# Kernel optimization log

Measured on AMD Instinct MI355X. Metric: run time of the kernel, lower is better.

## Reference

```python
import jax, jax.numpy as jnp
import numpy as np

NUM_HEADS = 4
KEY_DIM = 64
D_MODEL = 256
OUTPUT_DIM = 256


def setup_inputs() -> dict:
    key = jax.random.key(0)
    ks = jax.random.split(key, 11)
    B, T, D = 16, 1024, D_MODEL
    HD = NUM_HEADS * KEY_DIM
    s = 0.02
    return {
        "query": jax.random.normal(ks[0], (B, T, D), jnp.float32),
        "key": jax.random.normal(ks[1], (B, T, D), jnp.float32),
        "value": jax.random.normal(ks[2], (B, T, D), jnp.float32),
        "Wq": jax.random.normal(ks[3], (D, HD), jnp.float32) * s,
        "bq": jnp.zeros((HD,), jnp.float32),
        "Wk": jax.random.normal(ks[4], (D, HD), jnp.float32) * s,
        "bk": jnp.zeros((HD,), jnp.float32),
        "Wv": jax.random.normal(ks[5], (D, KEY_DIM), jnp.float32) * s,
        "bv": jnp.zeros((KEY_DIM,), jnp.float32),
        "Wo": jax.random.normal(ks[6], (HD, OUTPUT_DIM), jnp.float32) * s,
        "bo": jnp.zeros((OUTPUT_DIM,), jnp.float32),
    }


def reference(query, key, value, Wq, bq, Wk, bk, Wv, bv, Wo, bo):
    B, Tq, _ = query.shape
    Tk = key.shape[1]
    H, Dk = NUM_HEADS, KEY_DIM
    # projections
    q = (query @ Wq + bq).reshape(B, Tq, H, Dk)  # [B,Tq,H,Dk]
    k = (key @ Wk + bk).reshape(B, Tk, H, Dk)    # [B,Tk,H,Dk]
    v = value @ Wv + bv                           # [B,Tk,Dk] shared across heads
    scale = jnp.asarray(Dk, q.dtype) ** -0.5
    # scores [B,H,Tq,Tk]
    score = jnp.einsum("bqhd,bkhd->bhqk", q, k) * scale
    attn = jax.nn.softmax(score, axis=-1)
    # broadcast-V attention: [B,H,Tq,Tk] x [B,Tk,Dk] -> [B,H,Tq,Dk]
    out = jnp.einsum("bhqk,bkd->bhqd", attn, v)
    out = out.transpose(0, 2, 1, 3).reshape(B, Tq, H * Dk)
    return out @ Wo + bo
```

## Files before the change

### kernel.cpp

```cpp
#include <hip/hip_runtime.h>
#include <hip/hip_bf16.h>


typedef __attribute__((ext_vector_type(8))) short short8;
typedef __attribute__((ext_vector_type(4))) float f32x4;
typedef __attribute__((ext_vector_type(16))) float f32x16;

__device__ __forceinline__ short f2bf(float x) {
    return __builtin_bit_cast(short, __float2bfloat16(x));
}

__device__ __forceinline__ float exp2_fast(float x) {
#if __has_builtin(__builtin_amdgcn_exp2f)
    return __builtin_amdgcn_exp2f(x);
#else
    float r; asm("v_exp_f32 %0, %1" : "=v"(r) : "v"(x)); return r;
#endif
}

__device__ __forceinline__ f32x4 mfma16(short8 a, short8 b, f32x4 c) {
    return __builtin_amdgcn_mfma_f32_16x16x32_bf16(a, b, c, 0, 0, 0);
}
__device__ __forceinline__ f32x16 mfma32(short8 a, short8 b, f32x16 c) {
    return __builtin_amdgcn_mfma_f32_32x32x16_bf16(a, b, c, 0, 0, 0);
}

__device__ __forceinline__ int cvtpk(float lo, float hi) {
    int r; asm("v_cvt_pk_bf16_f32 %0, %1, %2" : "=v"(r) : "v"(lo), "v"(hi));
    return r;
}
__device__ __forceinline__ void swap32(int& a, int& b) {
    asm("v_permlane32_swap_b32 %0, %1" : "+v"(a), "+v"(b));
}

__device__ __forceinline__ short8 half_frag(const f32x16& s, int base) {
    int d0 = cvtpk(s[base + 0], s[base + 1]);
    int d1 = cvtpk(s[base + 2], s[base + 3]);
    int d2 = cvtpk(s[base + 4], s[base + 5]);
    int d3 = cvtpk(s[base + 6], s[base + 7]);
    swap32(d0, d2);
    swap32(d1, d3);
    int4 v = { d0, d1, d2, d3 };
    return __builtin_bit_cast(short8, v);
}

#define QSCALE 0.18033688011112042f

__global__ void prep_weights(const float* __restrict__ Wq, const float* __restrict__ Wk,
                             const float* __restrict__ Wv, const float* __restrict__ Wo,
                             short* __restrict__ WqtF, short* __restrict__ WktF,
                             short* __restrict__ WvtF, short* __restrict__ WotF) {
    int tid = blockIdx.x * 256 + threadIdx.x;
    int k = tid >> 8, n = tid & 255;
    int off = ((n >> 6) << 14) + (((n >> 4) & 3) << 12) + ((k >> 5) << 9)
            + (((k >> 3) & 3) << 7) + ((n & 15) << 3) + (k & 7);
    WqtF[off] = f2bf(Wq[k * 256 + n] * QSCALE);
    WktF[off] = f2bf(Wk[k * 256 + n]);
    int offo = ((n >> 5) << 13) + ((k >> 4) << 9) + (((k & 15) >> 3) << 8)
             + ((n & 31) << 3) + (k & 7);
    WotF[offo] = f2bf(Wo[k * 256 + n]);
    if (n < 64) {
        int offv = ((n >> 4) << 12) + ((k >> 5) << 9) + (((k >> 3) & 3) << 7)
                 + ((n & 15) << 3) + (k & 7);
        WvtF[offv] = f2bf(Wv[k * 64 + n]);
    }
}

__global__ __launch_bounds__(256) void proj_all(
        const float* __restrict__ query, const float* __restrict__ key_,
        const float* __restrict__ value,
        const short* __restrict__ WqtF, const short* __restrict__ WktF,
        const short* __restrict__ WvtF,
        const float* __restrict__ bq, const float* __restrict__ bk,
        const float* __restrict__ bv,
        short* __restrict__ qf, short* __restrict__ kf, short* __restrict__ vf) {
    __shared__ short At[8192];
    const int tid = threadIdx.x;
    const int lane = tid & 63, wave = tid >> 6;
    const int u = lane >> 4, r16 = lane & 15;
    const int m0 = blockIdx.x * 32;
    const int task = blockIdx.y;

    const float* A = task == 0 ? query : (task == 1 ? key_ : value);

    #pragma unroll
    for (int j = 0; j < 4; ++j) {
        int p8 = j * 8 + ((wave >> 1) << 2) + u;
        int row = ((wave & 1) << 4) + r16;
        const float* src = A + (m0 + row) * 256 + p8 * 8;
        float4 a0 = *(const float4*)src;
        float4 a1 = *(const float4*)(src + 4);
        short8 w;
        w[0] = f2bf(a0.x); w[1] = f2bf(a0.y); w[2] = f2bf(a0.z); w[3] = f2bf(a0.w);
        w[4] = f2bf(a1.x); w[5] = f2bf(a1.y); w[6] = f2bf(a1.z); w[7] = f2bf(a1.w);
        int dst = ((p8 >> 2) << 10) + ((wave & 1) << 9) + ((p8 & 3) << 7) + (r16 << 3);
        *(short8*)&At[dst] = w;
    }

    const int b = m0 >> 10, t32 = (m0 >> 5) & 31;

    if (task < 2) {
        const short* WtF = task == 0 ? WqtF : WktF;
        const float* bias = task == 0 ? bq : bk;
        const float bscale = task == 0 ? QSCALE : 1.0f;
        short* outF = task == 0 ? qf : kf;
        const short* wb = WtF + (wave << 14);

        short8 bf8[4];
        #pragma unroll
        for (int g = 0; g < 4; ++g) bf8[g] = *(const short8*)&wb[(g << 12) + lane * 8];
        __syncthreads();

        f32x4 acc[2][4] = {};
        #pragma unroll
        for (int kk = 0; kk < 8; ++kk) {
            short8 af[2], nb[4];
            #pragma unroll
            for (int f = 0; f < 2; ++f) af[f] = *(const short8*)&At[(kk << 10) + (f << 9) + lane * 8];
            if (kk < 7) {
                #pragma unroll
                for (int g = 0; g < 4; ++g) nb[g] = *(const short8*)&wb[(g << 12) + ((kk + 1) << 9) + lane * 8];
            }
            #pragma unroll
            for (int f = 0; f < 2; ++f)
                #pragma unroll
                for (int g = 0; g < 4; ++g)
                    acc[f][g] = mfma16(af[f], bf8[g], acc[f][g]);
            #pragma unroll
            for (int g = 0; g < 4; ++g) bf8[g] = nb[g];
        }

        float bvv[4];
        #pragma unroll
        for (int g = 0; g < 4; ++g) bvv[g] = bias[(wave << 6) + 16 * g + r16] * bscale;
        short* ob = outF + ((((b << 2) + wave) << 5) + t32) * 2048;
        #pragma unroll
        for (int f = 0; f < 2; ++f)
            #pragma unroll
            for (int g = 0; g < 4; ++g)
                #pragma unroll
                for (int rr = 0; rr < 4; ++rr)
                    ob[(g << 9) + ((r16 >> 3) << 8) + (16 * f + 4 * u + rr) * 8 + (r16 & 7)]
                        = f2bf(acc[f][g][rr] + bvv[g]);
    } else {
        const int fr = wave >> 1;
        short8 bf8[2];
        #pragma unroll
        for (int z = 0; z < 2; ++z) {
            int dg = ((wave & 1) << 1) + z;
            bf8[z] = *(const short8*)&WvtF[(dg << 12) + lane * 8];
        }
        __syncthreads();

        f32x4 acc[2] = {};
        #pragma unroll
        for (int kk = 0; kk < 8; ++kk) {
            short8 af = *(const short8*)&At[(kk << 10) + (fr << 9) + lane * 8];
            short8 nb[2];
            if (kk < 7) {
                #pragma unroll
                for (int z = 0; z < 2; ++z) {
                    int dg = ((wave & 1) << 1) + z;
                    nb[z] = *(const short8*)&WvtF[(dg << 12) + ((kk + 1) << 9) + lane * 8];
                }
            }
            #pragma unroll
            for (int z = 0; z < 2; ++z) acc[z] = mfma16(af, bf8[z], acc[z]);
            bf8[0] = nb[0]; bf8[1] = nb[1];
        }

        short* ob = vf + ((b << 5) + t32) * 2048;
        #pragma unroll
        for (int z = 0; z < 2; ++z) {
            int dg = ((wave & 1) << 1) + z;
            float bvv = bv[16 * dg + r16];
            #pragma unroll
            for (int rr = 0; rr < 4; ++rr) {
                int tl = 4 * u + rr;
                ob[((dg >> 1) << 10) + (fr << 9) + ((tl >> 3) << 8)
                   + ((16 * (dg & 1) + r16) << 3) + (tl & 7)]
                    = f2bf(acc[z][rr] + bvv);
            }
        }
    }
}

__global__ __launch_bounds__(256, 3) void attn_og(const short* __restrict__ qF,
        const short* __restrict__ kF, const short* __restrict__ vF,
        const short* __restrict__ WoF, const float* __restrict__ bo,
        float* __restrict__ outp) {
    __shared__ short At[8192];
    const int tid = threadIdx.x;
    const int lane = tid & 63, h = tid >> 6;
    const int u2 = lane >> 5, n31 = lane & 31;

    const int L = (blockIdx.x & 7) * 64 + (blockIdx.x >> 3);
    const int b = L >> 5, qt = L & 31;

    const short* qb = qF + ((((b << 2) + h) << 5) + qt) * 2048;
    short8 Q[4];
    #pragma unroll
    for (int c = 0; c < 4; ++c) Q[c] = *(const short8*)&qb[(c << 9) + lane * 8];

    const short* kb = kF + (((b << 2) + h) << 5) * 2048;
    const short* vb = vF + (b << 5) * 2048;

    short8 kfr[4], vfr[4];
    #pragma unroll
    for (int c = 0; c < 4; ++c) {
        kfr[c] = *(const short8*)&kb[(c << 9) + lane * 8];
        vfr[c] = *(const short8*)&vb[(c << 9) + lane * 8];
    }

    f32x16 accO0 = {}, accO1 = {};
    float l = 0.f;

    for (int kt = 0; kt < 32; ++kt) {
        short8 nk[4], nv[4];
        if (kt < 31) {
            const short* kn = kb + (kt + 1) * 2048;
            const short* vn = vb + (kt + 1) * 2048;
            #pragma unroll
            for (int c = 0; c < 4; ++c) {
                nk[c] = *(const short8*)&kn[(c << 9) + lane * 8];
                nv[c] = *(const short8*)&vn[(c << 9) + lane * 8];
            }
        }

        f32x16 S = {};
        __builtin_amdgcn_s_setprio(1);
        S = mfma32(kfr[0], Q[0], S);
        S = mfma32(kfr[1], Q[1], S);
        S = mfma32(kfr[2], Q[2], S);
        S = mfma32(kfr[3], Q[3], S);
        __builtin_amdgcn_s_setprio(0);

        f32x16 E;
        #pragma unroll
        for (int j = 0; j < 16; ++j) E[j] = exp2_fast(S[j]);
        l += (((E[0] + E[1]) + (E[2] + E[3])) + ((E[4] + E[5]) + (E[6] + E[7])))
           + (((E[8] + E[9]) + (E[10] + E[11])) + ((E[12] + E[13]) + (E[14] + E[15])));

        short8 p0 = half_frag(E, 0);
        short8 p1 = half_frag(E, 8);

        __builtin_amdgcn_s_setprio(1);
        accO0 = mfma32(vfr[0], p0, accO0);
        accO0 = mfma32(vfr[1], p1, accO0);
        accO1 = mfma32(vfr[2], p0, accO1);
        accO1 = mfma32(vfr[3], p1, accO1);
        __builtin_amdgcn_s_setprio(0);

        #pragma unroll
        for (int c = 0; c < 4; ++c) { kfr[c] = nk[c]; vfr[c] = nv[c]; }
    }

    l += __shfl_xor(l, 32);
    float linv = 1.0f / l;

    f32x16 O0, O1;
    #pragma unroll
    for (int j = 0; j < 16; ++j) { O0[j] = accO0[j] * linv; O1[j] = accO1[j] * linv; }
    {
        short8 a0 = half_frag(O0, 0), a1 = half_frag(O0, 8);
        short8 a2 = half_frag(O1, 0), a3 = half_frag(O1, 8);
        *(short8*)&At[((4 * h + 0) << 9) + lane * 8] = a0;
        *(short8*)&At[((4 * h + 1) << 9) + lane * 8] = a1;
        *(short8*)&At[((4 * h + 2) << 9) + lane * 8] = a2;
        *(short8*)&At[((4 * h + 3) << 9) + lane * 8] = a3;
    }
    __syncthreads();

    const short* wo0 = WoF + (2 * h) * 8192;
    const short* wo1 = wo0 + 8192;
    f32x16 acc2[2] = {};
    #pragma unroll
    for (int kc = 0; kc < 16; ++kc) {
        short8 a = *(const short8*)&At[(kc << 9) + lane * 8];
        short8 w0 = *(const short8*)&wo0[(kc << 9) + lane * 8];
        short8 w1 = *(const short8*)&wo1[(kc << 9) + lane * 8];
        acc2[0] = mfma32(a, w0, acc2[0]);
        acc2[1] = mfma32(a, w1, acc2[1]);
    }

    const int m0 = L << 5;
    #pragma unroll
    for (int nt2 = 0; nt2 < 2; ++nt2) {
        float bvv = bo[(2 * h + nt2) * 32 + n31];
        #pragma unroll
        for (int r = 0; r < 16; ++r) {
            int q = (r & 3) + 8 * (r >> 2) + 4 * u2;
            outp[(m0 + q) * 256 + (2 * h + nt2) * 32 + n31] = acc2[nt2][r] + bvv;
        }
    }
}

extern "C" void kernel_launch(void* const* d_in, const int* in_sizes, int n_in,
                              void* d_out, int out_size, void* d_ws, size_t ws_size,
                              hipStream_t stream) {
    (void)in_sizes; (void)n_in; (void)out_size; (void)ws_size;
    const float* query = (const float*)d_in[0];
    const float* key_  = (const float*)d_in[1];
    const float* value = (const float*)d_in[2];
    const float* Wq = (const float*)d_in[3];
    const float* bq = (const float*)d_in[4];
    const float* Wk = (const float*)d_in[5];
    const float* bk = (const float*)d_in[6];
    const float* Wv = (const float*)d_in[7];
    const float* bv = (const float*)d_in[8];
    const float* Wo = (const float*)d_in[9];
    const float* bo = (const float*)d_in[10];
    float* outp = (float*)d_out;

    short* wsp  = (short*)d_ws;
    short* WqtF = wsp;
    short* WktF = wsp + 65536;
    short* WotF = wsp + 131072;
    short* WvtF = wsp + 196608;
    short* qf   = wsp + 212992;
    short* kf   = wsp + 4407296;
    short* vf   = wsp + 8601600;

    hipLaunchKernelGGL(prep_weights, dim3(256), dim3(256), 0, stream,
                       Wq, Wk, Wv, Wo, WqtF, WktF, WvtF, WotF);
    hipLaunchKernelGGL(proj_all, dim3(512, 3), dim3(256), 0, stream,
                       query, key_, value, WqtF, WktF, WvtF, bq, bk, bv, qf, kf, vf);
    hipLaunchKernelGGL(attn_og, dim3(512), dim3(256), 0, stream,
                       qf, kf, vf, WotF, bo, outp);
}
```

Baseline: 55.29 us.

## Split KV range across wave pairs and process two query tiles per wave

Each block now covers 64 query rows with 512 threads. Every head gets two waves that each handle half of the key/value sequence over both query tiles, so each K/V fragment load feeds twice as many MFMAs. The partial outputs and row sums are merged through shared memory before the output projection, which is then split across all 8 waves. The cost is more LDS (about 100KB per block), an extra barrier and reduction step, and fewer blocks (256 instead of 512), which may leave many CUs underused. Softmax still uses no running max, as before.

```diff
diff --git a/kernel.cpp b/kernel.cpp
--- a/kernel.cpp
+++ b/kernel.cpp
@@ -42,6 +42,11 @@
     swap32(d1, d3);
     int4 v = { d0, d1, d2, d3 };
     return __builtin_bit_cast(short8, v);
+}
+
+__device__ __forceinline__ float sum16(const f32x16& e) {
+    return (((e[0] + e[1]) + (e[2] + e[3])) + ((e[4] + e[5]) + (e[6] + e[7])))
+         + (((e[8] + e[9]) + (e[10] + e[11])) + ((e[12] + e[13]) + (e[14] + e[15])));
 }
 
 #define QSCALE 0.18033688011112042f
@@ -185,25 +190,31 @@
     }
 }
 
-__global__ __launch_bounds__(256, 3) void attn_og(const short* __restrict__ qF,
+__global__ __launch_bounds__(512, 2) void attn_og(const short* __restrict__ qF,
         const short* __restrict__ kF, const short* __restrict__ vF,
         const short* __restrict__ WoF, const float* __restrict__ bo,
         float* __restrict__ outp) {
-    __shared__ short At[8192];
+    __shared__ float ocm[16384];
+    __shared__ float lcm[512];
+    __shared__ short At[16384];
     const int tid = threadIdx.x;
-    const int lane = tid & 63, h = tid >> 6;
+    const int lane = tid & 63, wave = tid >> 6;
+    const int h = wave >> 1, kvh = wave & 1;
     const int u2 = lane >> 5, n31 = lane & 31;
 
-    const int L = (blockIdx.x & 7) * 64 + (blockIdx.x >> 3);
-    const int b = L >> 5, qt = L & 31;
-
-    const short* qb = qF + ((((b << 2) + h) << 5) + qt) * 2048;
-    short8 Q[4];
+    const int L = (blockIdx.x & 7) * 32 + (blockIdx.x >> 3);
+    const int b = L >> 4, qt = L & 15;
+
+    const short* qb = qF + ((((b << 2) + h) << 5) + (qt << 1)) * 2048;
+    short8 Q0[4], Q1[4];
     #pragma unroll
-    for (int c = 0; c < 4; ++c) Q[c] = *(const short8*)&qb[(c << 9) + lane * 8];
-
-    const short* kb = kF + (((b << 2) + h) << 5) * 2048;
-    const short* vb = vF + (b << 5) * 2048;
+    for (int c = 0; c < 4; ++c) {
+        Q0[c] = *(const short8*)&qb[(c << 9) + lane * 8];
+        Q1[c] = *(const short8*)&qb[2048 + (c << 9) + lane * 8];
+    }
+
+    const short* kb = kF + ((((b << 2) + h) << 5) + (kvh << 4)) * 2048;
+    const short* vb = vF + (((b << 5) + (kvh << 4))) * 2048;
 
     short8 kfr[4], vfr[4];
     #pragma unroll
@@ -212,14 +223,14 @@
         vfr[c] = *(const short8*)&vb[(c << 9) + lane * 8];
     }
 
-    f32x16 accO0 = {}, accO1 = {};
-    float l = 0.f;
-
-    for (int kt = 0; kt < 32; ++kt) {
+    f32x16 aO00 = {}, aO01 = {}, aO10 = {}, aO11 = {};
+    float l0 = 0.f, l1 = 0.f;
+
+    for (int i = 0; i < 16; ++i) {
         short8 nk[4], nv[4];
-        if (kt < 31) {
-            const short* kn = kb + (kt + 1) * 2048;
-            const short* vn = vb + (kt + 1) * 2048;
+        if (i < 15) {
+            const short* kn = kb + (i + 1) * 2048;
+            const short* vn = vb + (i + 1) * 2048;
             #pragma unroll
             for (int c = 0; c < 4; ++c) {
                 nk[c] = *(const short8*)&kn[(c << 9) + lane * 8];
@@ -227,70 +238,119 @@
             }
         }
 
-        f32x16 S = {};
+        f32x16 S0 = {}, S1 = {};
         __builtin_amdgcn_s_setprio(1);
-        S = mfma32(kfr[0], Q[0], S);
-        S = mfma32(kfr[1], Q[1], S);
-        S = mfma32(kfr[2], Q[2], S);
-        S = mfma32(kfr[3], Q[3], S);
+        S0 = mfma32(kfr[0], Q0[0], S0); S1 = mfma32(kfr[0], Q1[0], S1);
+        S0 = mfma32(kfr[1], Q0[1], S0); S1 = mfma32(kfr[1], Q1[1], S1);
+        S0 = mfma32(kfr[2], Q0[2], S0); S1 = mfma32(kfr[2], Q1[2], S1);
+        S0 = mfma32(kfr[3], Q0[3], S0); S1 = mfma32(kfr[3], Q1[3], S1);
         __builtin_amdgcn_s_setprio(0);
 
-        f32x16 E;
-        #pragma unroll
-        for (int j = 0; j < 16; ++j) E[j] = exp2_fast(S[j]);
-        l += (((E[0] + E[1]) + (E[2] + E[3])) + ((E[4] + E[5]) + (E[6] + E[7])))
-           + (((E[8] + E[9]) + (E[10] + E[11])) + ((E[12] + E[13]) + (E[14] + E[15])));
-
-        short8 p0 = half_frag(E, 0);
-        short8 p1 = half_frag(E, 8);
+        #pragma unroll
+        for (int j = 0; j < 16; ++j) S0[j] = exp2_fast(S0[j]);
+        #pragma unroll
+        for (int j = 0; j < 16; ++j) S1[j] = exp2_fast(S1[j]);
+        l0 += sum16(S0);
+        l1 += sum16(S1);
+
+        short8 p00 = half_frag(S0, 0), p01 = half_frag(S0, 8);
+        short8 p10 = half_frag(S1, 0), p11 = half_frag(S1, 8);
 
         __builtin_amdgcn_s_setprio(1);
-        accO0 = mfma32(vfr[0], p0, accO0);
-        accO0 = mfma32(vfr[1], p1, accO0);
-        accO1 = mfma32(vfr[2], p0, accO1);
-        accO1 = mfma32(vfr[3], p1, accO1);
+        aO00 = mfma32(vfr[0], p00, aO00); aO00 = mfma32(vfr[1], p01, aO00);
+        aO10 = mfma32(vfr[2], p00, aO10); aO10 = mfma32(vfr[3], p01, aO10);
+        aO01 = mfma32(vfr[0], p10, aO01); aO01 = mfma32(vfr[1], p11, aO01);
+        aO11 = mfma32(vfr[2], p10, aO11); aO11 = mfma32(vfr[3], p11, aO11);
         __builtin_amdgcn_s_setprio(0);
 
         #pragma unroll
         for (int c = 0; c < 4; ++c) { kfr[c] = nk[c]; vfr[c] = nv[c]; }
     }
 
-    l += __shfl_xor(l, 32);
-    float linv = 1.0f / l;
-
-    f32x16 O0, O1;
-    #pragma unroll
-    for (int j = 0; j < 16; ++j) { O0[j] = accO0[j] * linv; O1[j] = accO1[j] * linv; }
-    {
-        short8 a0 = half_frag(O0, 0), a1 = half_frag(O0, 8);
-        short8 a2 = half_frag(O1, 0), a3 = half_frag(O1, 8);
-        *(short8*)&At[((4 * h + 0) << 9) + lane * 8] = a0;
-        *(short8*)&At[((4 * h + 1) << 9) + lane * 8] = a1;
-        *(short8*)&At[((4 * h + 2) << 9) + lane * 8] = a2;
-        *(short8*)&At[((4 * h + 3) << 9) + lane * 8] = a3;
+    l0 += __shfl_xor(l0, 32);
+    l1 += __shfl_xor(l1, 32);
+
+    float4* ocm4 = (float4*)ocm;
+    if (kvh == 1) {
+        #pragma unroll
+        for (int j4 = 0; j4 < 4; ++j4) {
+            float4 w0 = { aO00[4 * j4], aO00[4 * j4 + 1], aO00[4 * j4 + 2], aO00[4 * j4 + 3] };
+            float4 w1 = { aO10[4 * j4], aO10[4 * j4 + 1], aO10[4 * j4 + 2], aO10[4 * j4 + 3] };
+            float4 w2 = { aO01[4 * j4], aO01[4 * j4 + 1], aO01[4 * j4 + 2], aO01[4 * j4 + 3] };
+            float4 w3 = { aO11[4 * j4], aO11[4 * j4 + 1], aO11[4 * j4 + 2], aO11[4 * j4 + 3] };
+            ocm4[(((h << 2) + 0) * 4 + j4) * 64 + lane] = w0;
+            ocm4[(((h << 2) + 1) * 4 + j4) * 64 + lane] = w1;
+            ocm4[(((h << 2) + 2) * 4 + j4) * 64 + lane] = w2;
+            ocm4[(((h << 2) + 3) * 4 + j4) * 64 + lane] = w3;
+        }
+        lcm[(h << 1) * 64 + lane] = l0;
+        lcm[((h << 1) + 1) * 64 + lane] = l1;
     }
     __syncthreads();
 
-    const short* wo0 = WoF + (2 * h) * 8192;
+    if (kvh == 0) {
+        #pragma unroll
+        for (int j4 = 0; j4 < 4; ++j4) {
+            float4 r0 = ocm4[(((h << 2) + 0) * 4 + j4) * 64 + lane];
+            float4 r1 = ocm4[(((h << 2) + 1) * 4 + j4) * 64 + lane];
+            float4 r2 = ocm4[(((h << 2) + 2) * 4 + j4) * 64 + lane];
+            float4 r3 = ocm4[(((h << 2) + 3) * 4 + j4) * 64 + lane];
+            #pragma unroll
+            for (int e = 0; e < 4; ++e) {
+                aO00[4 * j4 + e] += ((const float*)&r0)[e];
+                aO10[4 * j4 + e] += ((const float*)&r1)[e];
+                aO01[4 * j4 + e] += ((const float*)&r2)[e];
+                aO11[4 * j4 + e] += ((const float*)&r3)[e];
+            }
+        }
+        float li0 = 1.0f / (l0 + lcm[(h << 1) * 64 + lane]);
+        float li1 = 1.0f / (l1 + lcm[((h << 1) + 1) * 64 + lane]);
+
+        #pragma unroll
+        for (int j = 0; j < 16; ++j) {
+            aO00[j] *= li0; aO10[j] *= li0;
+            aO01[j] *= li1; aO11[j] *= li1;
+        }
+
+        short8 a00 = half_frag(aO00, 0), a01 = half_frag(aO00, 8);
+        short8 a10 = half_frag(aO10, 0), a11 = half_frag(aO10, 8);
+        short8 b00 = half_frag(aO01, 0), b01 = half_frag(aO01, 8);
+        short8 b10 = half_frag(aO10, 0), b11 = half_frag(aO11, 8);
+        b10 = half_frag(aO11, 0);
+        *(short8*)&At[(((h << 2) + 0) << 9) + lane * 8] = a00;
+        *(short8*)&At[(((h << 2) + 1) << 9) + lane * 8] = a01;
+        *(short8*)&At[(((h << 2) + 2) << 9) + lane * 8] = a10;
+        *(short8*)&At[(((h << 2) + 3) << 9) + lane * 8] = a11;
+        *(short8*)&At[8192 + (((h << 2) + 0) << 9) + lane * 8] = b00;
+        *(short8*)&At[8192 + (((h << 2) + 1) << 9) + lane * 8] = b01;
+        *(short8*)&At[8192 + (((h << 2) + 2) << 9) + lane * 8] = b10;
+        *(short8*)&At[8192 + (((h << 2) + 3) << 9) + lane * 8] = b11;
+    }
+    __syncthreads();
+
+    const int qtile = wave >> 2, np = wave & 3;
+    const short* at = &At[qtile << 13];
+    const short* wo0 = WoF + (2 * np) * 8192;
     const short* wo1 = wo0 + 8192;
-    f32x16 acc2[2] = {};
+    f32x16 acc20 = {}, acc21 = {};
     #pragma unroll
     for (int kc = 0; kc < 16; ++kc) {
-        short8 a = *(const short8*)&At[(kc << 9) + lane * 8];
+        short8 a = *(const short8*)&at[(kc << 9) + lane * 8];
         short8 w0 = *(const short8*)&wo0[(kc << 9) + lane * 8];
         short8 w1 = *(const short8*)&wo1[(kc << 9) + lane * 8];
-        acc2[0] = mfma32(a, w0, acc2[0]);
-        acc2[1] = mfma32(a, w1, acc2[1]);
-    }
-
-    const int m0 = L << 5;
-    #pragma unroll
-    for (int nt2 = 0; nt2 < 2; ++nt2) {
-        float bvv = bo[(2 * h + nt2) * 32 + n31];
+        acc20 = mfma32(a, w0, acc20);
+        acc21 = mfma32(a, w1, acc21);
+    }
+
+    const int m0 = (L << 6) + (qtile << 5);
+    {
+        float bv0 = bo[(2 * np) * 32 + n31];
+        float bv1 = bo[(2 * np + 1) * 32 + n31];
         #pragma unroll
         for (int r = 0; r < 16; ++r) {
             int q = (r & 3) + 8 * (r >> 2) + 4 * u2;
-            outp[(m0 + q) * 256 + (2 * h + nt2) * 32 + n31] = acc2[nt2][r] + bvv;
+            outp[(m0 + q) * 256 + (2 * np) * 32 + n31] = acc20[r] + bv0;
+            outp[(m0 + q) * 256 + (2 * np + 1) * 32 + n31] = acc21[r] + bv1;
         }
     }
 }
@@ -325,6 +385,6 @@
                        Wq, Wk, Wv, Wo, WqtF, WktF, WvtF, WotF);
     hipLaunchKernelGGL(proj_all, dim3(512, 3), dim3(256), 0, stream,
                        query, key_, value, WqtF, WktF, WvtF, bq, bk, bv, qf, kf, vf);
-    hipLaunchKernelGGL(attn_og, dim3(512), dim3(256), 0, stream,
+    hipLaunchKernelGGL(attn_og, dim3(256), dim3(512), 0, stream,
                        qf, kf, vf, WotF, bo, outp);
 }
```

Result: faster. 53.57 us (-3.1%).

## Split key range across two wave groups per block and merge partial attention

Applied to the files above, without the earlier changes.

The attention kernel now launches 512 threads per block, with two wave groups each processing half of the 32 key tiles for the same query tile and head. Partial output accumulators and softmax denominators from the second group go through shared memory and are summed by the first before normalization. The output projection is spread across all 8 waves, one 32-column slice each. This doubles the waves per block to hide latency on a grid of only 512 blocks, at the cost of extra shared memory (about 48KB), an added barrier, and dropping the explicit next-tile prefetch of K/V.

```diff
diff --git a/kernel.cpp b/kernel.cpp
--- a/kernel.cpp
+++ b/kernel.cpp
@@ -42,6 +42,11 @@
     swap32(d1, d3);
     int4 v = { d0, d1, d2, d3 };
     return __builtin_bit_cast(short8, v);
+}
+
+__device__ __forceinline__ float sum16(const f32x16& e) {
+    return (((e[0] + e[1]) + (e[2] + e[3])) + ((e[4] + e[5]) + (e[6] + e[7])))
+         + (((e[8] + e[9]) + (e[10] + e[11])) + ((e[12] + e[13]) + (e[14] + e[15])));
 }
 
 #define QSCALE 0.18033688011112042f
@@ -185,13 +190,16 @@
     }
 }
 
-__global__ __launch_bounds__(256, 3) void attn_og(const short* __restrict__ qF,
+__global__ __launch_bounds__(512, 4) void attn_og(const short* __restrict__ qF,
         const short* __restrict__ kF, const short* __restrict__ vF,
         const short* __restrict__ WoF, const float* __restrict__ bo,
         float* __restrict__ outp) {
+    __shared__ float4 ocm4s[2048];
+    __shared__ float lcm[256];
     __shared__ short At[8192];
     const int tid = threadIdx.x;
-    const int lane = tid & 63, h = tid >> 6;
+    const int lane = tid & 63, wave = tid >> 6;
+    const int h = wave & 3, kvh = wave >> 2;
     const int u2 = lane >> 5, n31 = lane & 31;
 
     const int L = (blockIdx.x & 7) * 64 + (blockIdx.x >> 3);
@@ -202,29 +210,20 @@
     #pragma unroll
     for (int c = 0; c < 4; ++c) Q[c] = *(const short8*)&qb[(c << 9) + lane * 8];
 
-    const short* kb = kF + (((b << 2) + h) << 5) * 2048;
-    const short* vb = vF + (b << 5) * 2048;
-
-    short8 kfr[4], vfr[4];
-    #pragma unroll
-    for (int c = 0; c < 4; ++c) {
-        kfr[c] = *(const short8*)&kb[(c << 9) + lane * 8];
-        vfr[c] = *(const short8*)&vb[(c << 9) + lane * 8];
-    }
-
-    f32x16 accO0 = {}, accO1 = {};
+    const short* kb = kF + ((((b << 2) + h) << 5) + (kvh << 4)) * 2048;
+    const short* vb = vF + (((b << 5) + (kvh << 4))) * 2048;
+
+    f32x16 aO0 = {}, aO1 = {};
     float l = 0.f;
 
-    for (int kt = 0; kt < 32; ++kt) {
-        short8 nk[4], nv[4];
-        if (kt < 31) {
-            const short* kn = kb + (kt + 1) * 2048;
-            const short* vn = vb + (kt + 1) * 2048;
-            #pragma unroll
-            for (int c = 0; c < 4; ++c) {
-                nk[c] = *(const short8*)&kn[(c << 9) + lane * 8];
-                nv[c] = *(const short8*)&vn[(c << 9) + lane * 8];
-            }
+    for (int i = 0; i < 16; ++i) {
+        const short* kt = kb + i * 2048;
+        const short* vt = vb + i * 2048;
+        short8 kfr[4], vfr[4];
+        #pragma unroll
+        for (int c = 0; c < 4; ++c) {
+            kfr[c] = *(const short8*)&kt[(c << 9) + lane * 8];
+            vfr[c] = *(const short8*)&vt[(c << 9) + lane * 8];
         }
 
         f32x16 S = {};
@@ -235,62 +234,74 @@
         S = mfma32(kfr[3], Q[3], S);
         __builtin_amdgcn_s_setprio(0);
 
-        f32x16 E;
-        #pragma unroll
-        for (int j = 0; j < 16; ++j) E[j] = exp2_fast(S[j]);
-        l += (((E[0] + E[1]) + (E[2] + E[3])) + ((E[4] + E[5]) + (E[6] + E[7])))
-           + (((E[8] + E[9]) + (E[10] + E[11])) + ((E[12] + E[13]) + (E[14] + E[15])));
-
-        short8 p0 = half_frag(E, 0);
-        short8 p1 = half_frag(E, 8);
+        #pragma unroll
+        for (int j = 0; j < 16; ++j) S[j] = exp2_fast(S[j]);
+        l += sum16(S);
+
+        short8 p0 = half_frag(S, 0);
+        short8 p1 = half_frag(S, 8);
 
         __builtin_amdgcn_s_setprio(1);
-        accO0 = mfma32(vfr[0], p0, accO0);
-        accO0 = mfma32(vfr[1], p1, accO0);
-        accO1 = mfma32(vfr[2], p0, accO1);
-        accO1 = mfma32(vfr[3], p1, accO1);
+        aO0 = mfma32(vfr[0], p0, aO0);
+        aO0 = mfma32(vfr[1], p1, aO0);
+        aO1 = mfma32(vfr[2], p0, aO1);
+        aO1 = mfma32(vfr[3], p1, aO1);
         __builtin_amdgcn_s_setprio(0);
-
-        #pragma unroll
-        for (int c = 0; c < 4; ++c) { kfr[c] = nk[c]; vfr[c] = nv[c]; }
     }
 
     l += __shfl_xor(l, 32);
-    float linv = 1.0f / l;
-
-    f32x16 O0, O1;
-    #pragma unroll
-    for (int j = 0; j < 16; ++j) { O0[j] = accO0[j] * linv; O1[j] = accO1[j] * linv; }
-    {
-        short8 a0 = half_frag(O0, 0), a1 = half_frag(O0, 8);
-        short8 a2 = half_frag(O1, 0), a3 = half_frag(O1, 8);
-        *(short8*)&At[((4 * h + 0) << 9) + lane * 8] = a0;
-        *(short8*)&At[((4 * h + 1) << 9) + lane * 8] = a1;
-        *(short8*)&At[((4 * h + 2) << 9) + lane * 8] = a2;
-        *(short8*)&At[((4 * h + 3) << 9) + lane * 8] = a3;
+
+    if (kvh == 1) {
+        #pragma unroll
+        for (int j4 = 0; j4 < 4; ++j4) {
+            float4 w0 = { aO0[4 * j4], aO0[4 * j4 + 1], aO0[4 * j4 + 2], aO0[4 * j4 + 3] };
+            float4 w1 = { aO1[4 * j4], aO1[4 * j4 + 1], aO1[4 * j4 + 2], aO1[4 * j4 + 3] };
+            ocm4s[(((h << 1) + 0) * 4 + j4) * 64 + lane] = w0;
+            ocm4s[(((h << 1) + 1) * 4 + j4) * 64 + lane] = w1;
+        }
+        lcm[(h << 6) + lane] = l;
     }
     __syncthreads();
 
-    const short* wo0 = WoF + (2 * h) * 8192;
-    const short* wo1 = wo0 + 8192;
-    f32x16 acc2[2] = {};
+    if (kvh == 0) {
+        #pragma unroll
+        for (int j4 = 0; j4 < 4; ++j4) {
+            float4 r0 = ocm4s[(((h << 1) + 0) * 4 + j4) * 64 + lane];
+            float4 r1 = ocm4s[(((h << 1) + 1) * 4 + j4) * 64 + lane];
+            aO0[4 * j4 + 0] += r0.x; aO0[4 * j4 + 1] += r0.y;
+            aO0[4 * j4 + 2] += r0.z; aO0[4 * j4 + 3] += r0.w;
+            aO1[4 * j4 + 0] += r1.x; aO1[4 * j4 + 1] += r1.y;
+            aO1[4 * j4 + 2] += r1.z; aO1[4 * j4 + 3] += r1.w;
+        }
+        float li = 1.0f / (l + lcm[(h << 6) + lane]);
+        #pragma unroll
+        for (int j = 0; j < 16; ++j) { aO0[j] *= li; aO1[j] *= li; }
+
+        short8 a00 = half_frag(aO0, 0), a01 = half_frag(aO0, 8);
+        short8 a10 = half_frag(aO1, 0), a11 = half_frag(aO1, 8);
+        *(short8*)&At[(((h << 2) + 0) << 9) + lane * 8] = a00;
+        *(short8*)&At[(((h << 2) + 1) << 9) + lane * 8] = a01;
+        *(short8*)&At[(((h << 2) + 2) << 9) + lane * 8] = a10;
+        *(short8*)&At[(((h << 2) + 3) << 9) + lane * 8] = a11;
+    }
+    __syncthreads();
+
+    const short* wo0 = WoF + wave * 8192;
+    f32x16 acc2 = {};
     #pragma unroll
     for (int kc = 0; kc < 16; ++kc) {
         short8 a = *(const short8*)&At[(kc << 9) + lane * 8];
         short8 w0 = *(const short8*)&wo0[(kc << 9) + lane * 8];
-        short8 w1 = *(const short8*)&wo1[(kc << 9) + lane * 8];
-        acc2[0] = mfma32(a, w0, acc2[0]);
-        acc2[1] = mfma32(a, w1, acc2[1]);
+        acc2 = mfma32(a, w0, acc2);
     }
 
     const int m0 = L << 5;
-    #pragma unroll
-    for (int nt2 = 0; nt2 < 2; ++nt2) {
-        float bvv = bo[(2 * h + nt2) * 32 + n31];
+    {
+        float bv0 = bo[wave * 32 + n31];
         #pragma unroll
         for (int r = 0; r < 16; ++r) {
             int q = (r & 3) + 8 * (r >> 2) + 4 * u2;
-            outp[(m0 + q) * 256 + (2 * h + nt2) * 32 + n31] = acc2[nt2][r] + bvv;
+            outp[(m0 + q) * 256 + wave * 32 + n31] = acc2[r] + bv0;
         }
     }
 }
@@ -325,6 +336,6 @@
                        Wq, Wk, Wv, Wo, WqtF, WktF, WvtF, WotF);
     hipLaunchKernelGGL(proj_all, dim3(512, 3), dim3(256), 0, stream,
                        query, key_, value, WqtF, WktF, WvtF, bq, bk, bv, qf, kf, vf);
-    hipLaunchKernelGGL(attn_og, dim3(512), dim3(256), 0, stream,
+    hipLaunchKernelGGL(attn_og, dim3(512), dim3(512), 0, stream,
                        qf, kf, vf, WotF, bo, outp);
 }
```

Result: slower. 56.66 us (+2.5%).
